# Performance work log

Measured on AMD Instinct MI355X. Metric: run time of the kernel, lower is better.

Reference implementation:

```python
import jax, jax.numpy as jnp
import numpy as np

N_BALLS = 256
BATCH = 128
N_STEPS = 100
MAX_EVENTS = 5
WORLD_W = 10.0
WORLD_H = 10.0
RADIUS = 0.1
HID = 64
DT = 0.05
INF = jnp.float32(1e30)

_II_np, _JJ_np = np.triu_indices(N_BALLS, 1)
_II = jnp.asarray(_II_np)
_JJ = jnp.asarray(_JJ_np)
# wall order: left, right, bottom, top (normals point into the box)
_WN = jnp.array([[1.0, 0.0], [-1.0, 0.0], [0.0, 1.0], [0.0, -1.0]], dtype=jnp.float32)
_WP = jnp.array([0.0, -WORLD_W, 0.0, -WORLD_H], dtype=jnp.float32)


def setup_inputs():
    key = jax.random.key(0)
    ks = jax.random.split(key, 6)
    pos = jax.random.uniform(ks[0], (BATCH, N_BALLS, 2), minval=0.5, maxval=9.5)
    vel = jax.random.normal(ks[1], (BATCH, N_BALLS, 2))
    state = jnp.concatenate([pos, vel], axis=-1)  # [B, N, 4]
    radii = jnp.full((N_BALLS,), RADIUS, dtype=jnp.float32)
    sc = 0.1
    W1 = jax.random.normal(ks[2], (HID, 2)) * sc
    b1 = jnp.zeros((HID,), jnp.float32)
    W2 = jax.random.normal(ks[3], (HID, HID)) * sc
    b2 = jnp.zeros((HID,), jnp.float32)
    W3 = jax.random.normal(ks[4], (1, HID)) * sc
    b3 = jnp.zeros((1,), jnp.float32)
    return {"state": state, "radii": radii, "W1": W1, "b1": b1, "W2": W2,
            "b2": b2, "W3": W3, "b3": b3, "dt": DT, "n_steps": N_STEPS}


def _detect(pos, vel, radii):
    # pos, vel: [N,2]; vectorized replacement of the Python O(N^2) loop.
    diff = pos[_JJ] - pos[_II]                       # [P,2]
    dist = jnp.linalg.norm(diff, axis=-1)            # [P]
    gap_b = dist - (radii[_II] + radii[_JJ])
    nhat = diff / (dist + 1e-8)[:, None]
    app_b = jnp.sum((vel[_JJ] - vel[_II]) * nhat, axis=-1)
    gb = jnp.where(app_b < 0, gap_b, INF)            # only approaching pairs
    r = radii
    gw = jnp.stack([pos[:, 0] - r, WORLD_W - pos[:, 0] - r,
                    pos[:, 1] - r, WORLD_H - pos[:, 1] - r], axis=-1)  # [N,4]
    vw = jnp.stack([vel[:, 0] < 0, vel[:, 0] > 0,
                    vel[:, 1] < 0, vel[:, 1] > 0], axis=-1)
    gw = jnp.where(vw, gw, INF)
    allg = jnp.concatenate([gb, gw.reshape(-1)])
    k = jnp.argmin(allg)
    P = gb.shape[0]
    is_ball = k < P
    gap = allg[k]
    bi = jnp.where(is_ball, k, 0)
    i_b, j_b = _II[bi], _JJ[bi]
    kw = jnp.where(is_ball, 0, k - P)
    i_w, wid = kw // 4, kw % 4
    return gap, is_ball, i_b, j_b, i_w, wid


def _apply_jump(s, i, j, W1, b1, W2, b2, W3, b3):
    pos, vel = s[..., :2], s[..., 2:]
    diff = pos[:, j] - pos[:, i]                               # [B,2]
    dist = jnp.maximum(jnp.linalg.norm(diff, axis=-1, keepdims=True), 1e-8)
    nhat = diff / dist
    app = jnp.sum((vel[:, j] - vel[:, i]) * nhat, axis=-1, keepdims=True)
    h = jnp.concatenate([dist, app], axis=-1)                  # [B,2]
    h = jax.nn.silu(h @ W1.T + b1)
    h = jax.nn.silu(h @ W2.T + b2)
    imp = (h @ W3.T + b3) * nhat                               # [B,2]
    vel_new = vel.at[:, i].add(imp).at[:, j].add(-imp)
    return jnp.concatenate([pos, vel_new], axis=-1)


def _apply_wall(s, i, wn, wp, r):
    pos, vel = s[..., :2], s[..., 2:]
    v, p = vel[:, i], pos[:, i]
    vn = jnp.sum(v * wn, axis=-1, keepdims=True)
    vel_new = vel.at[:, i].set(v - 2.0 * vn * wn)
    pn = jnp.sum(p * wn, axis=-1, keepdims=True)
    pen = jnp.maximum(wp + r - pn, 0.0)
    pos_new = pos.at[:, i].set(p + pen * wn)
    return jnp.concatenate([pos_new, vel_new], axis=-1)


def _rollout(state, radii, W1, b1, W2, b2, W3, b3, dt, n_steps):
    dt = jnp.float32(dt)

    def event_body(_, carry):
        curr, t_c, t_e, done = carry
        pos0, vel0 = curr[0, :, :2], curr[0, :, 2:]
        gap, is_ball, i_b, j_b, i_w, wid = _detect(pos0, vel0, radii)
        no_event = gap > 0.05
        n = pos0[j_b] - pos0[i_b]
        app_ball = -jnp.sum((vel0[j_b] - vel0[i_b]) * n / jnp.linalg.norm(n))
        app_wall = jnp.abs(jnp.max(vel0[i_w]))
        app = jnp.where(is_ball, app_ball, app_wall)
        t_ev = t_c + gap / jnp.maximum(app, 1e-6)
        # ZeroFlow is constant velocity -> dopri5 integrate is exact linear drift
        dte = jnp.where(t_ev > t_c + 1e-10, t_ev - t_c, 0.0)

        def apply_map(s):
            jm = _apply_jump(s, i_b, j_b, W1, b1, W2, b2, W3, b3)
            wm = _apply_wall(s, i_w, _WN[wid], _WP[wid], radii[i_w])
            return jnp.where(is_ball, jm, wm)

        state_a = apply_map(curr)                       # gap <= 0: jump now
        integ = curr.at[..., :2].add(curr[..., 2:] * dte)
        state_b = apply_map(integ)                      # 0 < gap: drift then jump
        act = (~done) & (~no_event)
        case_a = act & (gap <= 0)
        case_b = act & (gap > 0) & (app > 1e-6) & (t_ev < t_e)
        new_done = done | no_event | (act & (gap > 0) & ((app <= 1e-6) | (t_ev >= t_e)))
        new_curr = jnp.where(case_a, state_a, jnp.where(case_b, state_b, curr))
        new_t_c = jnp.where(case_b, t_ev, t_c)
        return new_curr, new_t_c, t_e, new_done

    def step(curr, step_idx):
        t_s = step_idx.astype(jnp.float32) * dt
        t_e = t_s + dt
        curr, t_c, _, _ = jax.lax.fori_loop(
            0, MAX_EVENTS, event_body, (curr, t_s, t_e, jnp.bool_(False)))
        dte = jnp.where(t_e > t_c + 1e-10, t_e - t_c, 0.0)
        curr = curr.at[..., :2].add(curr[..., 2:] * dte)
        return curr, curr

    _, traj = jax.lax.scan(step, state, jnp.arange(n_steps))
    return jnp.concatenate([state[None], traj], axis=0)   # [n_steps+1, B, N, 4]


def reference(state, radii, W1, b1, W2, b2, W3, b3, dt, n_steps):
    return _rollout(state, radii, W1, b1, W2, b2, W3, b3, dt, n_steps)
```

## Files before the change

kernel.cpp:

```cpp
#include <hip/hip_runtime.h>
#include <stdint.h>

#define NB 256
#define NBATCH 128
#define HID 64
#define MAXEV 5
#define MAXSTEPS 256
#define NT 43
#define NTILES 946
#define W2S 65
#define CAND_MAX 6144
#define CMARGIN 1.5f

__device__ __forceinline__ float bf2f(unsigned short u) {
    return __uint_as_float(((unsigned)u) << 16);
}
__device__ __forceinline__ unsigned short f2bf(float f) {
    unsigned u = __float_as_uint(f);
    u += 0x7FFFu + ((u >> 16) & 1u);
    return (unsigned short)(u >> 16);
}
__device__ __forceinline__ float rdin(const void* p, int idx, int bf) {
    return bf ? bf2f(((const unsigned short*)p)[idx]) : ((const float*)p)[idx];
}
__device__ __forceinline__ float silu_f(float x) {
    float s = __fdiv_rn(1.0f, __fadd_rn(1.0f, expf(-x)));
    return __fmul_rn(x, s);
}
__device__ __forceinline__ void lds_fence() {
    __builtin_amdgcn_wave_barrier();
    __threadfence_block();
    __builtin_amdgcn_wave_barrier();
}
__device__ __forceinline__ unsigned long long shfl_down_u64(unsigned long long v, int off) {
    unsigned lo = (unsigned)v, hi = (unsigned)(v >> 32);
    lo = __shfl_down(lo, off);
    hi = __shfl_down(hi, off);
    return (((unsigned long long)hi) << 32) | lo;
}

__device__ void load_weights(float* w1, float* b1s, float* w2, float* b2s, float* w3, float* b3s,
                             const void* W1, const void* B1, const void* W2, const void* B2,
                             const void* W3, const void* B3, int bf, int tid, int nthr) {
    for (int k = tid; k < HID * 2; k += nthr) w1[k] = rdin(W1, k, bf);
    for (int k = tid; k < HID; k += nthr) {
        b1s[k] = rdin(B1, k, bf);
        b2s[k] = rdin(B2, k, bf);
        w3[k]  = rdin(W3, k, bf);
    }
    for (int k = tid; k < HID * HID; k += nthr) {
        int m = k >> 6, c = k & 63;
        w2[m * W2S + c] = rdin(W2, k, bf);
    }
    if (tid == 0) b3s[0] = rdin(B3, 0, bf);
}

__device__ __forceinline__ void pair_min(const float4* ps, int i, int j, unsigned long long& kP) {
    float4 A = ps[i], B = ps[j];
    float dx = __fsub_rn(B.x, A.x), dy = __fsub_rn(B.y, A.y);
    float d2 = __fadd_rn(__fmul_rn(dx, dx), __fmul_rn(dy, dy));
    float p1 = __fmul_rn(__fsub_rn(B.z, A.z), dx);
    float p2 = __fmul_rn(__fsub_rn(B.w, A.w), dy);
    float dot = __fadd_rn(p1, p2);
    float mag = __fadd_rn(fabsf(p1), fabsf(p2));
    bool appr;
    if (fabsf(dot) < __fmul_rn(1e-5f, mag)) {
        float dist = __fsqrt_rn(d2);
        float den = __fadd_rn(dist, 1e-8f);
        float ab = __fadd_rn(__fmul_rn(__fsub_rn(B.z, A.z), __fdiv_rn(dx, den)),
                             __fmul_rn(__fsub_rn(B.w, A.w), __fdiv_rn(dy, den)));
        appr = ab < 0.0f;
    } else {
        appr = dot < 0.0f;
    }
    if (appr) {
        unsigned long long key = (((unsigned long long)__float_as_uint(d2)) << 16) |
                                 (unsigned)((i << 8) | j);
        kP = key < kP ? key : kP;
    }
}

__global__ void sniff_kernel(const unsigned short* st, int* ws) {
    __shared__ int ev;
    if (threadIdx.x == 0) ev = 0;
    __syncthreads();
    unsigned short u = st[threadIdx.x];
    int e = (u >> 7) & 0xFF;
    if (e >= 0x85) atomicOr(&ev, 1);
    __syncthreads();
    if (threadIdx.x == 0) ws[0] = ev ? 0 : 1;
}

__global__ void row0_kernel(const void* in, void* out, const int* ws) {
    int idx = blockIdx.x * blockDim.x + threadIdx.x;
    if (ws[0]) ((unsigned short*)out)[idx] = ((const unsigned short*)in)[idx];
    else       ((float*)out)[idx] = ((const float*)in)[idx];
}

__global__ __launch_bounds__(1024, 1) void sim_kernel(
    const void* in_state, const void* in_rad,
    const void* inW1, const void* inB1, const void* inW2, const void* inB2,
    const void* inW3, const void* inB3, const void* in_dt, const int* in_nsteps,
    void* out, const int* ws) {
    __shared__ float4 ps0[NB];
    __shared__ float4 psb[NB];
    __shared__ float rad[NB];
    __shared__ float w1[HID * 2], b1s[HID], w2[HID * W2S], b2s[HID], w3s[HID], b3s[1];
    __shared__ float sc0[132], scb[132];
    __shared__ unsigned long long redP[16], redW[16];
    __shared__ float redF[4];
    __shared__ unsigned cand[CAND_MAX];
    __shared__ int candN;
    __shared__ int dI[4];
    __shared__ float dF[4];
    __shared__ int candF;
    __shared__ int rebF;

    int tid = threadIdx.x;
    int b = blockIdx.x;
    int bf = ws[0];

    if (tid < NB) {
        int base0 = tid * 4;
        float4 P;
        P.x = rdin(in_state, base0 + 0, bf);
        P.y = rdin(in_state, base0 + 1, bf);
        P.z = rdin(in_state, base0 + 2, bf);
        P.w = rdin(in_state, base0 + 3, bf);
        ps0[tid] = P;
        int baseb = (b * NB + tid) * 4;
        float4 Q;
        Q.x = rdin(in_state, baseb + 0, bf);
        Q.y = rdin(in_state, baseb + 1, bf);
        Q.z = rdin(in_state, baseb + 2, bf);
        Q.w = rdin(in_state, baseb + 3, bf);
        psb[tid] = Q;
        rad[tid] = rdin(in_rad, tid, bf);
        float m2 = P.z * P.z + P.w * P.w;
        #pragma unroll
        for (int off = 32; off; off >>= 1) m2 = fmaxf(m2, __shfl_down(m2, off));
        if ((tid & 63) == 0) redF[tid >> 6] = m2;
    }
    load_weights(w1, b1s, w2, b2s, w3s, b3s, inW1, inB1, inW2, inB2, inW3, inB3, bf, tid, 1024);
    if (tid == 0) { candN = 0; candF = 0; rebF = 1; }

    float dtv = rdin(in_dt, 0, bf);
    int NS = in_nsteps[0]; if (NS > MAXSTEPS) NS = MAXSTEPS; if (NS < 0) NS = 0;

    int myI0 = -1, myJ0 = 0;
    if (tid < NTILES) {
        int rem = tid, r = 0;
        while (rem >= NT - r) { rem -= NT - r; r++; }
        myI0 = r * 6; myJ0 = (r + rem) * 6;
    }
    __syncthreads();
    float rsum = __fadd_rn(rad[0], rad[0]);

    float theta = __fadd_rn(__fadd_rn(rsum, 0.05f), CMARGIN);
    float th2 = __fmul_rn(theta, theta);

    int nc = 0;
    bool candOvf = false;
    float used = 1e30f, vcap = 0.0f;

    for (int s = 0; s < NS; s++) {
        int rebuild = rebF;
        float t_s = __fmul_rn((float)s, dtv);
        float t_e = __fadd_rn(t_s, dtv);
        float t_c = t_s;
        if (tid < 64) {
            if (rebuild) {
                vcap = sqrtf(fmaxf(fmaxf(redF[0], redF[1]), fmaxf(redF[2], redF[3])));
                used = 0.0f;
            }
            used = __fadd_rn(used, __fmul_rn(__fmul_rn(2.0f, dtv), vcap));
            if (tid == 0 && rebuild) candF = 0;
        }

        for (int e = 0; e < MAXEV; e++) {
            unsigned long long kP = ~0ull, kW = ~0ull;
            bool fullscan = (e == 0) ? (rebuild != 0) : (candF != 0);
            bool doAppend = (e == 0) && rebuild;
            if (fullscan) {
                if (myI0 >= 0) {
                    float4 Pi[6], Pj[6];
                    #pragma unroll
                    for (int a = 0; a < 6; a++) {
                        int ii = myI0 + a; ii = ii < NB ? ii : NB - 1;
                        int jj = myJ0 + a; jj = jj < NB ? jj : NB - 1;
                        Pi[a] = ps0[ii]; Pj[a] = ps0[jj];
                    }
                    #pragma unroll
                    for (int a = 0; a < 6; a++) {
                        int i = myI0 + a;
                        #pragma unroll
                        for (int bb = 0; bb < 6; bb++) {
                            int j = myJ0 + bb;
                            bool ok = (i < NB) && (j < NB) && (j > i);
                            float dx = __fsub_rn(Pj[bb].x, Pi[a].x);
                            float dy = __fsub_rn(Pj[bb].y, Pi[a].y);
                            float d2 = __fadd_rn(__fmul_rn(dx, dx), __fmul_rn(dy, dy));
                            float p1 = __fmul_rn(__fsub_rn(Pj[bb].z, Pi[a].z), dx);
                            float p2 = __fmul_rn(__fsub_rn(Pj[bb].w, Pi[a].w), dy);
                            float dot = __fadd_rn(p1, p2);
                            float mag = __fadd_rn(fabsf(p1), fabsf(p2));
                            bool appr;
                            if (fabsf(dot) < __fmul_rn(1e-5f, mag)) {
                                float dist = __fsqrt_rn(d2);
                                float den = __fadd_rn(dist, 1e-8f);
                                float ab = __fadd_rn(
                                    __fmul_rn(__fsub_rn(Pj[bb].z, Pi[a].z), __fdiv_rn(dx, den)),
                                    __fmul_rn(__fsub_rn(Pj[bb].w, Pi[a].w), __fdiv_rn(dy, den)));
                                appr = ab < 0.0f;
                            } else {
                                appr = dot < 0.0f;
                            }
                            if (ok && appr) {
                                unsigned long long key =
                                    (((unsigned long long)__float_as_uint(d2)) << 16) |
                                    (unsigned)((i << 8) | j);
                                kP = key < kP ? key : kP;
                            }
                            if (doAppend && ok && d2 < th2) {
                                int x = atomicAdd(&candN, 1);
                                if (x < CAND_MAX) cand[x] = (unsigned)((i << 8) | j);
                            }
                        }
                    }
                }
            } else {
                for (int c = tid; c < nc; c += 1024) {
                    unsigned id = cand[c];
                    pair_min(ps0, (int)(id >> 8), (int)(id & 255u), kP);
                }
            }
            {
                int ball = tid >> 2, w = tid & 3;
                float4 P = ps0[ball]; float r = rad[ball];
                float g; bool valid;
                if (w == 0)      { g = __fsub_rn(P.x, r); valid = P.z < 0.0f; }
                else if (w == 1) { g = __fsub_rn(__fsub_rn(10.0f, P.x), r); valid = P.z > 0.0f; }
                else if (w == 2) { g = __fsub_rn(P.y, r); valid = P.w < 0.0f; }
                else             { g = __fsub_rn(__fsub_rn(10.0f, P.y), r); valid = P.w > 0.0f; }
                if (valid) {
                    unsigned gb = __float_as_uint(g);
                    unsigned m = (unsigned)(((int)gb) >> 31) | 0x80000000u;
                    unsigned sb = gb ^ m;
                    unsigned long long key = (((unsigned long long)sb) << 16) | (unsigned)tid;
                    kW = key < kW ? key : kW;
                }
            }
            #pragma unroll
            for (int off = 32; off; off >>= 1) {
                unsigned long long o1 = shfl_down_u64(kP, off);
                unsigned long long o2 = shfl_down_u64(kW, off);
                kP = o1 < kP ? o1 : kP;
                kW = o2 < kW ? o2 : kW;
            }
            if ((tid & 63) == 0) { redP[tid >> 6] = kP; redW[tid >> 6] = kW; }
            __syncthreads();

            if (e == 0 && rebuild) {
                int ct = candN;
                candOvf = ct > CAND_MAX;
                nc = candOvf ? CAND_MAX : ct;
            }

            float g_nx = 0, g_ny = 0, g_dist = 0, g_app = 0;
            float4 gA, gB;
            if (tid < 64) {
                unsigned long long mP = redP[0], mW = redW[0];
                #pragma unroll
                for (int q = 1; q < 16; q++) {
                    mP = redP[q] < mP ? redP[q] : mP;
                    mW = redW[q] < mW ? redW[q] : mW;
                }
                float gball = 1e30f; int pi = 0, pj = 1;
                if (mP != ~0ull) {
                    unsigned id = (unsigned)(mP & 0xFFFFull);
                    pi = id >> 8; pj = id & 255u;
                    float d2 = __uint_as_float((unsigned)(mP >> 16));
                    gball = __fsub_rn(__fsqrt_rn(d2), rsum);
                }
                float gwall = 1e30f; int wb = 0, ww = 0;
                if (mW != ~0ull) {
                    unsigned id = (unsigned)(mW & 0xFFFFull);
                    wb = id >> 2; ww = id & 3u;
                    unsigned sb = (unsigned)(mW >> 16);
                    unsigned gb = (sb & 0x80000000u) ? (sb ^ 0x80000000u) : ~sb;
                    gwall = __uint_as_float(gb);
                }
                bool is_ball = gball <= gwall;
                float gap = is_ball ? gball : gwall;
                int code_ = 0; float dteB_ = 0.0f, tcn_ = t_c;
                if (!(gap > 0.05f)) {
                    float app;
                    if (is_ball) {
                        float4 A = ps0[pi], B = ps0[pj];
                        float dx = __fsub_rn(B.x, A.x), dy = __fsub_rn(B.y, A.y);
                        float nrm = __fsqrt_rn(__fadd_rn(__fmul_rn(dx, dx), __fmul_rn(dy, dy)));
                        float dvx = __fsub_rn(B.z, A.z), dvy = __fsub_rn(B.w, A.w);
                        app = -__fadd_rn(__fdiv_rn(__fmul_rn(dvx, dx), nrm),
                                         __fdiv_rn(__fmul_rn(dvy, dy), nrm));
                    } else {
                        float4 Wb = ps0[wb];
                        app = fabsf(fmaxf(Wb.z, Wb.w));
                    }
                    float t_ev = __fadd_rn(t_c, __fdiv_rn(gap, fmaxf(app, 1e-6f)));
                    if (gap <= 0.0f) {
                        code_ = is_ball ? 1 : 3;
                    } else if (app > 1e-6f && t_ev < t_e) {
                        code_ = is_ball ? 2 : 4;
                        dteB_ = (t_ev > __fadd_rn(t_c, 1e-10f)) ? __fsub_rn(t_ev, t_c) : 0.0f;
                        tcn_ = t_ev;
                    }
                }
                int ei_ = is_ball ? pi : wb;
                int ej_ = is_ball ? pj : ww;
                if (tid == 0) {
                    dI[0] = code_; dI[1] = ei_; dI[2] = ej_;
                    dF[0] = dteB_; dF[1] = tcn_;
                }
                if (code_ != 0 && code_ <= 2) {
                    float4 A = ps0[ei_], B = ps0[ej_];
                    if (code_ == 2) {
                        A.x = __fadd_rn(A.x, __fmul_rn(A.z, dteB_));
                        A.y = __fadd_rn(A.y, __fmul_rn(A.w, dteB_));
                        B.x = __fadd_rn(B.x, __fmul_rn(B.z, dteB_));
                        B.y = __fadd_rn(B.y, __fmul_rn(B.w, dteB_));
                    }
                    gA = A; gB = B;
                    float dx = __fsub_rn(B.x, A.x), dy = __fsub_rn(B.y, A.y);
                    float nrm = __fsqrt_rn(__fadd_rn(__fmul_rn(dx, dx), __fmul_rn(dy, dy)));
                    float dist = fmaxf(nrm, 1e-8f);
                    g_nx = __fdiv_rn(dx, dist); g_ny = __fdiv_rn(dy, dist);
                    g_dist = dist;
                    float dvx = __fsub_rn(B.z, A.z), dvy = __fsub_rn(B.w, A.w);
                    g_app = __fadd_rn(__fmul_rn(dvx, g_nx), __fmul_rn(dvy, g_ny));
                }
            }
            __syncthreads();

            int code = dI[0];
            if (code == 0) break;
            int ei = dI[1], ejw = dI[2];
            float dteB = dF[0];
            t_c = dF[1];
            bool integ = (code == 2) || (code == 4);

            if (code <= 2) {
                if (tid < 64) {
                    float a = __fadd_rn(__fadd_rn(__fmul_rn(g_dist, w1[2 * tid]),
                                                  __fmul_rn(g_app, w1[2 * tid + 1])), b1s[tid]);
                    sc0[4 + tid] = silu_f(a);
                    lds_fence();
                    float acc = 0.0f;
                    const float* row = &w2[tid * W2S];
                    #pragma unroll 8
                    for (int k = 0; k < HID; k++) acc = __fadd_rn(acc, __fmul_rn(sc0[4 + k], row[k]));
                    acc = __fadd_rn(acc, b2s[tid]);
                    sc0[68 + tid] = silu_f(acc);
                    lds_fence();
                    float acc3 = 0.0f;
                    #pragma unroll 8
                    for (int k = 0; k < HID; k++)
                        acc3 = __fadd_rn(acc3, __fmul_rn(sc0[68 + k], w3s[k]));
                    float impv = __fadd_rn(acc3, b3s[0]);
                    float ix = __fmul_rn(impv, g_nx), iy = __fmul_rn(impv, g_ny);
                    float nAz = __fadd_rn(gA.z, ix),  nAw = __fadd_rn(gA.w, iy);
                    float nBz = __fadd_rn(gB.z, -ix), nBw = __fadd_rn(gB.w, -iy);
                    if (tid == 0) {
                        float4 outA; outA.x = gA.x; outA.y = gA.y; outA.z = nAz; outA.w = nAw;
                        float4 outB; outB.x = gB.x; outB.y = gB.y; outB.z = nBz; outB.w = nBw;
                        ps0[ei] = outA; ps0[ejw] = outB;
                    }
                    float s1 = sqrtf(nAz * nAz + nAw * nAw);
                    float s2 = sqrtf(nBz * nBz + nBw * nBw);
                    float nv = fmaxf(s1, s2);
                    used = __fadd_rn(used, __fmul_rn(__fmul_rn(2.0f, dtv),
                                                     fmaxf(__fsub_rn(nv, vcap), 0.0f)));
                    vcap = fmaxf(vcap, nv);
                    int nf = (candOvf || (__fadd_rn(used, 1e-3f) > CMARGIN)) ? 1 : 0;
                    if (tid == 0) candF = nf;
                } else if (tid < 128) {
                    int lane = tid - 64;
                    float4 A = psb[ei], B = psb[ejw];
                    if (integ) {
                        A.x = __fadd_rn(A.x, __fmul_rn(A.z, dteB));
                        A.y = __fadd_rn(A.y, __fmul_rn(A.w, dteB));
                        B.x = __fadd_rn(B.x, __fmul_rn(B.z, dteB));
                        B.y = __fadd_rn(B.y, __fmul_rn(B.w, dteB));
                    }
                    float dx = __fsub_rn(B.x, A.x), dy = __fsub_rn(B.y, A.y);
                    float nrm = __fsqrt_rn(__fadd_rn(__fmul_rn(dx, dx), __fmul_rn(dy, dy)));
                    float dist = fmaxf(nrm, 1e-8f);
                    float nx = __fdiv_rn(dx, dist), ny = __fdiv_rn(dy, dist);
                    float dvx = __fsub_rn(B.z, A.z), dvy = __fsub_rn(B.w, A.w);
                    float app2 = __fadd_rn(__fmul_rn(dvx, nx), __fmul_rn(dvy, ny));
                    float a = __fadd_rn(__fadd_rn(__fmul_rn(dist, w1[2 * lane]),
                                                  __fmul_rn(app2, w1[2 * lane + 1])), b1s[lane]);
                    scb[4 + lane] = silu_f(a);
                    lds_fence();
                    float acc = 0.0f;
                    const float* row = &w2[lane * W2S];
                    #pragma unroll 8
                    for (int k = 0; k < HID; k++) acc = __fadd_rn(acc, __fmul_rn(scb[4 + k], row[k]));
                    acc = __fadd_rn(acc, b2s[lane]);
                    scb[68 + lane] = silu_f(acc);
                    lds_fence();
                    float acc3 = 0.0f;
                    #pragma unroll 8
                    for (int k = 0; k < HID; k++)
                        acc3 = __fadd_rn(acc3, __fmul_rn(scb[68 + k], w3s[k]));
                    float impv = __fadd_rn(acc3, b3s[0]);
                    if (lane == 0) {
                        float ix = __fmul_rn(impv, nx), iy = __fmul_rn(impv, ny);
                        float4 outA; outA.x = A.x; outA.y = A.y;
                        outA.z = __fadd_rn(A.z, ix);  outA.w = __fadd_rn(A.w, iy);
                        float4 outB; outB.x = B.x; outB.y = B.y;
                        outB.z = __fadd_rn(B.z, -ix); outB.w = __fadd_rn(B.w, -iy);
                        psb[ei] = outA; psb[ejw] = outB;
                    }
                } else if (tid < 384) {
                    int t = tid - 128;
                    if (integ && t != ei && t != ejw) {
                        float4 P = ps0[t];
                        P.x = __fadd_rn(P.x, __fmul_rn(P.z, dteB));
                        P.y = __fadd_rn(P.y, __fmul_rn(P.w, dteB));
                        ps0[t] = P;
                    }
                } else if (tid < 640) {
                    int t = tid - 384;
                    if (integ && t != ei && t != ejw) {
                        float4 Q = psb[t];
                        Q.x = __fadd_rn(Q.x, __fmul_rn(Q.z, dteB));
                        Q.y = __fadd_rn(Q.y, __fmul_rn(Q.w, dteB));
                        psb[t] = Q;
                    }
                }
                __syncthreads();
            } else {
                const float wnx[4] = {1.f, -1.f, 0.f, 0.f};
                const float wny[4] = {0.f, 0.f, 1.f, -1.f};
                const float wpv[4] = {0.f, -10.f, 0.f, -10.f};
                int w = ejw;
                if (tid < 64) {
                    float4 P = ps0[ei];
                    if (integ) {
                        P.x = __fadd_rn(P.x, __fmul_rn(P.z, dteB));
                        P.y = __fadd_rn(P.y, __fmul_rn(P.w, dteB));
                    }
                    float vn = __fadd_rn(__fmul_rn(P.z, wnx[w]), __fmul_rn(P.w, wny[w]));
                    float t2 = __fmul_rn(2.0f, vn);
                    float nvx = __fsub_rn(P.z, __fmul_rn(t2, wnx[w]));
                    float nvy = __fsub_rn(P.w, __fmul_rn(t2, wny[w]));
                    float pn = __fadd_rn(__fmul_rn(P.x, wnx[w]), __fmul_rn(P.y, wny[w]));
                    float pen = fmaxf(__fsub_rn(__fadd_rn(wpv[w], rad[ei]), pn), 0.0f);
                    float4 nP;
                    nP.x = __fadd_rn(P.x, __fmul_rn(pen, wnx[w]));
                    nP.y = __fadd_rn(P.y, __fmul_rn(pen, wny[w]));
                    nP.z = nvx; nP.w = nvy;
                    used = __fadd_rn(used, pen);
                    int nf = (candOvf || (__fadd_rn(used, 1e-3f) > CMARGIN)) ? 1 : 0;
                    if (tid == 0) { ps0[ei] = nP; candF = nf; }
                } else if (tid < 128) {
                    if (tid == 64) {
                        float4 P = psb[ei];
                        if (integ) {
                            P.x = __fadd_rn(P.x, __fmul_rn(P.z, dteB));
                            P.y = __fadd_rn(P.y, __fmul_rn(P.w, dteB));
                        }
                        float vn = __fadd_rn(__fmul_rn(P.z, wnx[w]), __fmul_rn(P.w, wny[w]));
                        float t2 = __fmul_rn(2.0f, vn);
                        float nvx = __fsub_rn(P.z, __fmul_rn(t2, wnx[w]));
                        float nvy = __fsub_rn(P.w, __fmul_rn(t2, wny[w]));
                        float pn = __fadd_rn(__fmul_rn(P.x, wnx[w]), __fmul_rn(P.y, wny[w]));
                        float pen = fmaxf(__fsub_rn(__fadd_rn(wpv[w], rad[ei]), pn), 0.0f);
                        float4 nP;
                        nP.x = __fadd_rn(P.x, __fmul_rn(pen, wnx[w]));
                        nP.y = __fadd_rn(P.y, __fmul_rn(pen, wny[w]));
                        nP.z = nvx; nP.w = nvy;
                        psb[ei] = nP;
                    }
                } else if (tid < 384) {
                    int t = tid - 128;
                    if (integ && t != ei) {
                        float4 P = ps0[t];
                        P.x = __fadd_rn(P.x, __fmul_rn(P.z, dteB));
                        P.y = __fadd_rn(P.y, __fmul_rn(P.w, dteB));
                        ps0[t] = P;
                    }
                } else if (tid < 640) {
                    int t = tid - 384;
                    if (integ && t != ei) {
                        float4 Q = psb[t];
                        Q.x = __fadd_rn(Q.x, __fmul_rn(Q.z, dteB));
                        Q.y = __fadd_rn(Q.y, __fmul_rn(Q.w, dteB));
                        psb[t] = Q;
                    }
                }
                __syncthreads();
            }
        }

        float fd = (t_e > __fadd_rn(t_c, 1e-10f)) ? __fsub_rn(t_e, t_c) : 0.0f;
        if (tid < NB) {
            float4 P = ps0[tid];
            P.x = __fadd_rn(P.x, __fmul_rn(P.z, fd));
            P.y = __fadd_rn(P.y, __fmul_rn(P.w, fd));
            ps0[tid] = P;
            float m2 = P.z * P.z + P.w * P.w;
            #pragma unroll
            for (int off = 32; off; off >>= 1) m2 = fmaxf(m2, __shfl_down(m2, off));
            if ((tid & 63) == 0) redF[tid >> 6] = m2;
            if (tid == 0) {
                candN = 0;
                float usedNext = __fadd_rn(used, __fmul_rn(__fmul_rn(2.0f, dtv), vcap));
                rebF = (candOvf || (__fadd_rn(usedNext, 1e-3f) > CMARGIN)) ? 1 : 0;
            }
        } else if (tid < 2 * NB) {
            int t = tid - NB;
            float4 Q = psb[t];
            Q.x = __fadd_rn(Q.x, __fmul_rn(Q.z, fd));
            Q.y = __fadd_rn(Q.y, __fmul_rn(Q.w, fd));
            psb[t] = Q;
            long long base = ((long long)(s + 1) * NBATCH + b) * (NB * 4);
            if (bf) {
                ushort4 v;
                v.x = f2bf(Q.x); v.y = f2bf(Q.y); v.z = f2bf(Q.z); v.w = f2bf(Q.w);
                ((ushort4*)((unsigned short*)out + base))[t] = v;
            } else {
                ((float4*)((float*)out + base))[t] = Q;
            }
        }
        __syncthreads();
    }
}

extern "C" void kernel_launch(void* const* d_in, const int* in_sizes, int n_in,
                              void* d_out, int out_size, void* d_ws, size_t ws_size,
                              hipStream_t stream) {
    int* ws = (int*)d_ws;
    sniff_kernel<<<1, 256, 0, stream>>>((const unsigned short*)d_in[0], ws);
    row0_kernel<<<(NBATCH * NB * 4) / 256, 256, 0, stream>>>(d_in[0], d_out, ws);
    sim_kernel<<<NBATCH, 1024, 0, stream>>>(
        d_in[0], d_in[1], d_in[2], d_in[3], d_in[4], d_in[5], d_in[6], d_in[7],
        d_in[8], (const int*)d_in[9], d_out, ws);
}
```

Before: 3.330 ms.

## Add tight per-step neighbor list and DPP wave reductions with aggregated appends

Adds a second, tighter candidate list (TMARGIN) built each step from the loose list or the full scan, so later events within a step scan fewer pairs. It also gates the approach test on a distance threshold, replaces shuffle-based wave reductions with DPP row operations plus readlane, and uses wave-aggregated atomics for list appends. This reduces per-event pair work and LDS atomic contention, at the cost of extra LDS, more per-event bookkeeping, and extra work in the event-0 pass that builds the tight list.

```diff
diff --git a/kernel.cpp b/kernel.cpp
--- a/kernel.cpp
+++ b/kernel.cpp
@@ -10,7 +10,9 @@
 #define NTILES 946
 #define W2S 65
 #define CAND_MAX 6144
+#define T_MAX 2048
 #define CMARGIN 1.5f
+#define TMARGIN 0.9f
 
 __device__ __forceinline__ float bf2f(unsigned short u) {
     return __uint_as_float(((unsigned)u) << 16);
@@ -32,11 +34,51 @@
     __threadfence_block();
     __builtin_amdgcn_wave_barrier();
 }
-__device__ __forceinline__ unsigned long long shfl_down_u64(unsigned long long v, int off) {
-    unsigned lo = (unsigned)v, hi = (unsigned)(v >> 32);
-    lo = __shfl_down(lo, off);
-    hi = __shfl_down(hi, off);
-    return (((unsigned long long)hi) << 32) | lo;
+
+template<int CTRL>
+__device__ __forceinline__ unsigned long long dpp_min_u64_step(unsigned long long k) {
+    unsigned lo = (unsigned)k, hi = (unsigned)(k >> 32);
+    unsigned nlo = (unsigned)__builtin_amdgcn_update_dpp(-1, (int)lo, CTRL, 0xF, 0xF, false);
+    unsigned nhi = (unsigned)__builtin_amdgcn_update_dpp(-1, (int)hi, CTRL, 0xF, 0xF, false);
+    unsigned long long nk = (((unsigned long long)nhi) << 32) | (unsigned long long)nlo;
+    return nk < k ? nk : k;
+}
+__device__ __forceinline__ unsigned long long wave_min_u64(unsigned long long k) {
+    k = dpp_min_u64_step<0x111>(k);
+    k = dpp_min_u64_step<0x112>(k);
+    k = dpp_min_u64_step<0x114>(k);
+    k = dpp_min_u64_step<0x118>(k);
+    k = dpp_min_u64_step<0x142>(k);
+    k = dpp_min_u64_step<0x143>(k);
+    unsigned lo = (unsigned)__builtin_amdgcn_readlane((int)(unsigned)k, 63);
+    unsigned hi = (unsigned)__builtin_amdgcn_readlane((int)(unsigned)(k >> 32), 63);
+    return (((unsigned long long)hi) << 32) | (unsigned long long)lo;
+}
+template<int CTRL>
+__device__ __forceinline__ float dpp_max_f32_step(float x) {
+    int nx = __builtin_amdgcn_update_dpp(0, __float_as_int(x), CTRL, 0xF, 0xF, false);
+    return fmaxf(x, __int_as_float(nx));
+}
+__device__ __forceinline__ float wave_max_f32(float x) {
+    x = dpp_max_f32_step<0x111>(x);
+    x = dpp_max_f32_step<0x112>(x);
+    x = dpp_max_f32_step<0x114>(x);
+    x = dpp_max_f32_step<0x118>(x);
+    x = dpp_max_f32_step<0x142>(x);
+    x = dpp_max_f32_step<0x143>(x);
+    return __int_as_float(__builtin_amdgcn_readlane(__float_as_int(x), 63));
+}
+
+__device__ __forceinline__ void append_agg(unsigned* list, int* counter, int cap, unsigned val) {
+    unsigned long long m = __ballot(1);
+    int lane = (int)(threadIdx.x & 63);
+    int ldr = (int)__builtin_ctzll(m);
+    int pfx = (int)__builtin_popcountll(m & ((1ull << lane) - 1ull));
+    int base = 0;
+    if (lane == ldr) base = atomicAdd(counter, (int)__builtin_popcountll(m));
+    base = __builtin_amdgcn_readfirstlane(base);
+    int idx = base + pfx;
+    if (idx < cap) list[idx] = val;
 }
 
 __device__ void load_weights(float* w1, float* b1s, float* w2, float* b2s, float* w3, float* b3s,
@@ -55,31 +97,6 @@
     if (tid == 0) b3s[0] = rdin(B3, 0, bf);
 }
 
-__device__ __forceinline__ void pair_min(const float4* ps, int i, int j, unsigned long long& kP) {
-    float4 A = ps[i], B = ps[j];
-    float dx = __fsub_rn(B.x, A.x), dy = __fsub_rn(B.y, A.y);
-    float d2 = __fadd_rn(__fmul_rn(dx, dx), __fmul_rn(dy, dy));
-    float p1 = __fmul_rn(__fsub_rn(B.z, A.z), dx);
-    float p2 = __fmul_rn(__fsub_rn(B.w, A.w), dy);
-    float dot = __fadd_rn(p1, p2);
-    float mag = __fadd_rn(fabsf(p1), fabsf(p2));
-    bool appr;
-    if (fabsf(dot) < __fmul_rn(1e-5f, mag)) {
-        float dist = __fsqrt_rn(d2);
-        float den = __fadd_rn(dist, 1e-8f);
-        float ab = __fadd_rn(__fmul_rn(__fsub_rn(B.z, A.z), __fdiv_rn(dx, den)),
-                             __fmul_rn(__fsub_rn(B.w, A.w), __fdiv_rn(dy, den)));
-        appr = ab < 0.0f;
-    } else {
-        appr = dot < 0.0f;
-    }
-    if (appr) {
-        unsigned long long key = (((unsigned long long)__float_as_uint(d2)) << 16) |
-                                 (unsigned)((i << 8) | j);
-        kP = key < kP ? key : kP;
-    }
-}
-
 __global__ void sniff_kernel(const unsigned short* st, int* ws) {
     __shared__ int ev;
     if (threadIdx.x == 0) ev = 0;
@@ -110,10 +127,12 @@
     __shared__ unsigned long long redP[16], redW[16];
     __shared__ float redF[4];
     __shared__ unsigned cand[CAND_MAX];
-    __shared__ int candN;
+    __shared__ unsigned cand2[T_MAX];
+    __shared__ int candN, candN2;
     __shared__ int dI[4];
     __shared__ float dF[4];
     __shared__ int candF;
+    __shared__ int candFt;
     __shared__ int rebF;
 
     int tid = threadIdx.x;
@@ -137,12 +156,11 @@
         psb[tid] = Q;
         rad[tid] = rdin(in_rad, tid, bf);
         float m2 = P.z * P.z + P.w * P.w;
-        #pragma unroll
-        for (int off = 32; off; off >>= 1) m2 = fmaxf(m2, __shfl_down(m2, off));
+        m2 = wave_max_f32(m2);
         if ((tid & 63) == 0) redF[tid >> 6] = m2;
     }
     load_weights(w1, b1s, w2, b2s, w3s, b3s, inW1, inB1, inW2, inB2, inW3, inB3, bf, tid, 1024);
-    if (tid == 0) { candN = 0; candF = 0; rebF = 1; }
+    if (tid == 0) { candN = 0; candN2 = 0; candF = 0; candFt = 0; rebF = 1; }
 
     float dtv = rdin(in_dt, 0, bf);
     int NS = in_nsteps[0]; if (NS > MAXSTEPS) NS = MAXSTEPS; if (NS < 0) NS = 0;
@@ -156,12 +174,14 @@
     __syncthreads();
     float rsum = __fadd_rn(rad[0], rad[0]);
 
-    float theta = __fadd_rn(__fadd_rn(rsum, 0.05f), CMARGIN);
-    float th2 = __fmul_rn(theta, theta);
-
-    int nc = 0;
-    bool candOvf = false;
-    float used = 1e30f, vcap = 0.0f;
+    float thB = __fadd_rn(__fadd_rn(rsum, 0.05f), CMARGIN);
+    float th2B = __fmul_rn(thB, thB);
+    float thT = __fadd_rn(__fadd_rn(rsum, 0.05f), TMARGIN);
+    float th2T = __fmul_rn(thT, thT);
+
+    int nc = 0, ncT = 0;
+    bool candOvf = false, tOvf = false;
+    float used = 1e30f, usedT = 0.0f, vcap = 0.0f;
 
     for (int s = 0; s < NS; s++) {
         int rebuild = rebF;
@@ -173,15 +193,21 @@
                 vcap = sqrtf(fmaxf(fmaxf(redF[0], redF[1]), fmaxf(redF[2], redF[3])));
                 used = 0.0f;
             }
-            used = __fadd_rn(used, __fmul_rn(__fmul_rn(2.0f, dtv), vcap));
-            if (tid == 0 && rebuild) candF = 0;
+            float pre = __fmul_rn(__fmul_rn(2.0f, dtv), vcap);
+            used = __fadd_rn(used, pre);
+            usedT = pre;
+            if (tid == 0) { if (rebuild) candF = 0; candFt = 0; }
         }
 
         for (int e = 0; e < MAXEV; e++) {
             unsigned long long kP = ~0ull, kW = ~0ull;
-            bool fullscan = (e == 0) ? (rebuild != 0) : (candF != 0);
-            bool doAppend = (e == 0) && rebuild;
-            if (fullscan) {
+            int mode;
+            if (e == 0) mode = rebuild ? 2 : 1;
+            else       mode = candF ? 2 : (candFt ? 1 : 0);
+            bool apT = (e == 0);
+
+            if (mode == 2) {
+                bool apB = apT;
                 if (myI0 >= 0) {
                     float4 Pi[6], Pj[6];
                     #pragma unroll
@@ -200,38 +226,70 @@
                             float dx = __fsub_rn(Pj[bb].x, Pi[a].x);
                             float dy = __fsub_rn(Pj[bb].y, Pi[a].y);
                             float d2 = __fadd_rn(__fmul_rn(dx, dx), __fmul_rn(dy, dy));
-                            float p1 = __fmul_rn(__fsub_rn(Pj[bb].z, Pi[a].z), dx);
-                            float p2 = __fmul_rn(__fsub_rn(Pj[bb].w, Pi[a].w), dy);
-                            float dot = __fadd_rn(p1, p2);
-                            float mag = __fadd_rn(fabsf(p1), fabsf(p2));
-                            bool appr;
-                            if (fabsf(dot) < __fmul_rn(1e-5f, mag)) {
-                                float dist = __fsqrt_rn(d2);
-                                float den = __fadd_rn(dist, 1e-8f);
-                                float ab = __fadd_rn(
-                                    __fmul_rn(__fsub_rn(Pj[bb].z, Pi[a].z), __fdiv_rn(dx, den)),
-                                    __fmul_rn(__fsub_rn(Pj[bb].w, Pi[a].w), __fdiv_rn(dy, den)));
-                                appr = ab < 0.0f;
-                            } else {
-                                appr = dot < 0.0f;
+                            unsigned id = (unsigned)((i << 8) | j);
+                            bool nearT = ok && (d2 < th2T);
+                            if (nearT) {
+                                float p1 = __fmul_rn(__fsub_rn(Pj[bb].z, Pi[a].z), dx);
+                                float p2 = __fmul_rn(__fsub_rn(Pj[bb].w, Pi[a].w), dy);
+                                float dot = __fadd_rn(p1, p2);
+                                float mag = __fadd_rn(fabsf(p1), fabsf(p2));
+                                bool appr;
+                                if (fabsf(dot) < __fmul_rn(1e-5f, mag)) {
+                                    float dist = __fsqrt_rn(d2);
+                                    float den = __fadd_rn(dist, 1e-8f);
+                                    float ab = __fadd_rn(
+                                        __fmul_rn(__fsub_rn(Pj[bb].z, Pi[a].z), __fdiv_rn(dx, den)),
+                                        __fmul_rn(__fsub_rn(Pj[bb].w, Pi[a].w), __fdiv_rn(dy, den)));
+                                    appr = ab < 0.0f;
+                                } else {
+                                    appr = dot < 0.0f;
+                                }
+                                if (appr) {
+                                    unsigned long long key =
+                                        (((unsigned long long)__float_as_uint(d2)) << 16) | id;
+                                    kP = key < kP ? key : kP;
+                                }
                             }
-                            if (ok && appr) {
-                                unsigned long long key =
-                                    (((unsigned long long)__float_as_uint(d2)) << 16) |
-                                    (unsigned)((i << 8) | j);
-                                kP = key < kP ? key : kP;
-                            }
-                            if (doAppend && ok && d2 < th2) {
-                                int x = atomicAdd(&candN, 1);
-                                if (x < CAND_MAX) cand[x] = (unsigned)((i << 8) | j);
+                            if (apB) {
+                                if (nearT) append_agg(cand2, &candN2, T_MAX, id);
+                                if (ok && d2 < th2B) append_agg(cand, &candN, CAND_MAX, id);
                             }
                         }
                     }
                 }
             } else {
-                for (int c = tid; c < nc; c += 1024) {
-                    unsigned id = cand[c];
-                    pair_min(ps0, (int)(id >> 8), (int)(id & 255u), kP);
+                const unsigned* src = (mode == 1) ? cand : cand2;
+                int n = (mode == 1) ? nc : ncT;
+                bool apT2 = apT && (mode == 1);
+                for (int c = tid; c < n; c += 1024) {
+                    unsigned id = src[c];
+                    int i = (int)(id >> 8), j = (int)(id & 255u);
+                    float4 A = ps0[i], B = ps0[j];
+                    float dx = __fsub_rn(B.x, A.x), dy = __fsub_rn(B.y, A.y);
+                    float d2 = __fadd_rn(__fmul_rn(dx, dx), __fmul_rn(dy, dy));
+                    if (d2 < th2T) {
+                        float p1 = __fmul_rn(__fsub_rn(B.z, A.z), dx);
+                        float p2 = __fmul_rn(__fsub_rn(B.w, A.w), dy);
+                        float dot = __fadd_rn(p1, p2);
+                        float mag = __fadd_rn(fabsf(p1), fabsf(p2));
+                        bool appr;
+                        if (fabsf(dot) < __fmul_rn(1e-5f, mag)) {
+                            float dist = __fsqrt_rn(d2);
+                            float den = __fadd_rn(dist, 1e-8f);
+                            float ab = __fadd_rn(
+                                __fmul_rn(__fsub_rn(B.z, A.z), __fdiv_rn(dx, den)),
+                                __fmul_rn(__fsub_rn(B.w, A.w), __fdiv_rn(dy, den)));
+                            appr = ab < 0.0f;
+                        } else {
+                            appr = dot < 0.0f;
+                        }
+                        if (appr) {
+                            unsigned long long key =
+                                (((unsigned long long)__float_as_uint(d2)) << 16) | id;
+                            kP = key < kP ? key : kP;
+                        }
+                        if (apT2) append_agg(cand2, &candN2, T_MAX, id);
+                    }
                 }
             }
             {
@@ -250,20 +308,20 @@
                     kW = key < kW ? key : kW;
                 }
             }
-            #pragma unroll
-            for (int off = 32; off; off >>= 1) {
-                unsigned long long o1 = shfl_down_u64(kP, off);
-                unsigned long long o2 = shfl_down_u64(kW, off);
-                kP = o1 < kP ? o1 : kP;
-                kW = o2 < kW ? o2 : kW;
-            }
+            kP = wave_min_u64(kP);
+            kW = wave_min_u64(kW);
             if ((tid & 63) == 0) { redP[tid >> 6] = kP; redW[tid >> 6] = kW; }
             __syncthreads();
 
-            if (e == 0 && rebuild) {
-                int ct = candN;
-                candOvf = ct > CAND_MAX;
-                nc = candOvf ? CAND_MAX : ct;
+            if (e == 0) {
+                if (rebuild) {
+                    int ct = candN;
+                    candOvf = ct > CAND_MAX;
+                    nc = candOvf ? CAND_MAX : ct;
+                }
+                int ct2 = candN2;
+                tOvf = ct2 > T_MAX;
+                ncT = tOvf ? T_MAX : ct2;
             }
 
             float g_nx = 0, g_ny = 0, g_dist = 0, g_app = 0;
@@ -377,11 +435,14 @@
                     float s1 = sqrtf(nAz * nAz + nAw * nAw);
                     float s2 = sqrtf(nBz * nBz + nBw * nBw);
                     float nv = fmaxf(s1, s2);
-                    used = __fadd_rn(used, __fmul_rn(__fmul_rn(2.0f, dtv),
-                                                     fmaxf(__fsub_rn(nv, vcap), 0.0f)));
+                    float delta = __fmul_rn(__fmul_rn(2.0f, dtv),
+                                            fmaxf(__fsub_rn(nv, vcap), 0.0f));
+                    used = __fadd_rn(used, delta);
+                    usedT = __fadd_rn(usedT, delta);
                     vcap = fmaxf(vcap, nv);
-                    int nf = (candOvf || (__fadd_rn(used, 1e-3f) > CMARGIN)) ? 1 : 0;
-                    if (tid == 0) candF = nf;
+                    int nf  = (candOvf || (__fadd_rn(used, 1e-3f) > CMARGIN)) ? 1 : 0;
+                    int nft = (tOvf || (__fadd_rn(usedT, 1e-3f) > TMARGIN)) ? 1 : 0;
+                    if (tid == 0) { candF = nf; candFt = nft; }
                 } else if (tid < 128) {
                     int lane = tid - 64;
                     float4 A = psb[ei], B = psb[ejw];
@@ -461,8 +522,10 @@
                     nP.y = __fadd_rn(P.y, __fmul_rn(pen, wny[w]));
                     nP.z = nvx; nP.w = nvy;
                     used = __fadd_rn(used, pen);
-                    int nf = (candOvf || (__fadd_rn(used, 1e-3f) > CMARGIN)) ? 1 : 0;
-                    if (tid == 0) { ps0[ei] = nP; candF = nf; }
+                    usedT = __fadd_rn(usedT, pen);
+                    int nf  = (candOvf || (__fadd_rn(used, 1e-3f) > CMARGIN)) ? 1 : 0;
+                    int nft = (tOvf || (__fadd_rn(usedT, 1e-3f) > TMARGIN)) ? 1 : 0;
+                    if (tid == 0) { ps0[ei] = nP; candF = nf; candFt = nft; }
                 } else if (tid < 128) {
                     if (tid == 64) {
                         float4 P = psb[ei];
@@ -510,11 +573,10 @@
             P.y = __fadd_rn(P.y, __fmul_rn(P.w, fd));
             ps0[tid] = P;
             float m2 = P.z * P.z + P.w * P.w;
-            #pragma unroll
-            for (int off = 32; off; off >>= 1) m2 = fmaxf(m2, __shfl_down(m2, off));
+            m2 = wave_max_f32(m2);
             if ((tid & 63) == 0) redF[tid >> 6] = m2;
             if (tid == 0) {
-                candN = 0;
+                candN = 0; candN2 = 0;
                 float usedNext = __fadd_rn(used, __fmul_rn(__fmul_rn(2.0f, dtv), vcap));
                 rebF = (candOvf || (__fadd_rn(usedNext, 1e-3f) > CMARGIN)) ? 1 : 0;
             }
```

New measurement: 3.642 ms. 9.4% more time.
